# Performance work log

Hardware: AMD Instinct MI355X
Metric: run time of the kernel (lower is better)

## Reference

```python
import jax, jax.numpy as jnp
import numpy as np

D = 1024
H = 16
HD = D // H          # 64
D2 = D // 2          # 512
B = 2
N = 1024


def setup_inputs() -> dict:
    key = jax.random.key(0)
    ks = jax.random.split(key, 12)
    std = 0.02
    init_std = 0.02 / np.sqrt(D)  # matches _init_weights for value/output proj
    return {
        "h": jax.random.normal(ks[0], (B, N, D), jnp.float32),
        "prev_idx": jax.random.randint(ks[1], (B, N), 0, N),
        # forward encoders: Linear(d, d/2) -> GELU -> Linear(d/2, 1), stacked over heads
        "fw_W1": jax.random.normal(ks[2], (H, D2, D), jnp.float32) * std,
        "fw_b1": jnp.zeros((H, D2), jnp.float32),
        "fw_W2": jax.random.normal(ks[3], (H, D2), jnp.float32) * std,  # out-dim 1 squeezed
        "fw_b2": jnp.zeros((H,), jnp.float32),
        # backward encoders
        "bw_W1": jax.random.normal(ks[4], (H, D2, D), jnp.float32) * std,
        "bw_b1": jnp.zeros((H, D2), jnp.float32),
        "bw_W2": jax.random.normal(ks[5], (H, D2), jnp.float32) * std,
        "bw_b2": jnp.zeros((H,), jnp.float32),
        # per-head value projection Linear(d, head_dim, bias=False)
        "Wv": jax.random.normal(ks[6], (H, HD, D), jnp.float32) * init_std,
        # relation fusion: Linear(3*hd, hd) -> GELU -> Linear(hd, hd)
        "fu_W1": jax.random.normal(ks[7], (H, HD, 3 * HD), jnp.float32) * std,
        "fu_b1": jnp.zeros((H, HD), jnp.float32),
        "fu_W2": jax.random.normal(ks[8], (H, HD, HD), jnp.float32) * std,
        "fu_b2": jnp.zeros((H, HD), jnp.float32),
        # output projection Linear(d, d, bias=False)
        "Wo": jax.random.normal(ks[9], (D, D), jnp.float32) * init_std,
        "chain_ratio": jnp.float32(0.5),
    }


def _encoder_logits(h, W1, b1, W2, b2):
    # h: [B,N,D]; W1: [H,D2,D]; returns [H,B,N]
    x = jnp.einsum('bnd,hkd->hbnk', h, W1) + b1[:, None, None, :]
    x = jax.nn.gelu(x, approximate=False)  # torch nn.GELU default = exact erf
    return jnp.einsum('hbnk,hk->hbn', x, W2) + b2[:, None, None]


def reference(h, prev_idx, fw_W1, fw_b1, fw_W2, fw_b2,
              bw_W1, bw_b1, bw_W2, bw_b2,
              Wv, fu_W1, fu_b1, fu_W2, fu_b2, Wo, chain_ratio):
    pos = jnp.arange(N, dtype=h.dtype)

    fwd_logits = _encoder_logits(h, fw_W1, fw_b1, fw_W2, fw_b2)  # [H,B,N]
    bwd_logits = _encoder_logits(h, bw_W1, bw_b1, bw_W2, bw_b2)  # [H,B,N]

    # faithful to original: softmax over an N-wise expansion of a scalar logit
    fwd_probs = jax.nn.softmax(
        jnp.broadcast_to(fwd_logits[..., None], (H, B, N, N)), axis=-1)
    bwd_probs = jax.nn.softmax(
        jnp.broadcast_to(bwd_logits[..., None], (H, B, N, N)), axis=-1)

    fwd_targets = jnp.sum(fwd_probs * pos, axis=-1).astype(jnp.int32)  # [H,B,N]
    bwd_targets = jnp.sum(bwd_probs * pos, axis=-1).astype(jnp.int32)

    # chaining with prev_idx (prev_idx is given)
    chain_threshold = jnp.floor(jax.nn.sigmoid(chain_ratio) * N)
    should_chain = jnp.arange(N) >= chain_threshold  # [N]
    prev_clamped = jnp.clip(prev_idx, 0, N - 1).astype(jnp.int32)  # [B,N]
    fwd_targets = jnp.where(should_chain[None, None, :],
                            prev_clamped[None, :, :], fwd_targets)

    head_features = jnp.einsum('bnd,hed->hbne', h, Wv)  # [H,B,N,HD]
    fwd_feats = jnp.einsum('hbnm,hbme->hbne', fwd_probs, head_features)
    bwd_feats = jnp.einsum('hbnm,hbme->hbne', bwd_probs, head_features)

    rel = jnp.concatenate([head_features, fwd_feats, bwd_feats], axis=-1)  # [H,B,N,3HD]
    x = jax.nn.gelu(jnp.einsum('hbnc,hec->hbne', rel, fu_W1)
                    + fu_b1[:, None, None, :], approximate=False)
    head_out = jnp.einsum('hbne,hfe->hbnf', x, fu_W2) + fu_b2[:, None, None, :]

    multi = jnp.transpose(head_out, (1, 2, 0, 3)).reshape(B, N, D)
    final_output = jnp.einsum('bnd,ed->bne', multi, Wo)

    eps = 1e-8
    fwd_strength = 1.0 - jnp.sum(fwd_probs * jnp.log(fwd_probs + eps), axis=-1)
    bwd_strength = 1.0 - jnp.sum(bwd_probs * jnp.log(bwd_probs + eps), axis=-1)
    avg_strength = jnp.mean((fwd_strength + bwd_strength) * 0.5, axis=0)  # [B,N]

    return (final_output, fwd_targets[0], bwd_targets[0], avg_strength)
```

## Files before the change

kernel.cpp:

```cpp
#include <hip/hip_runtime.h>
#include <hip/hip_bf16.h>


typedef __attribute__((ext_vector_type(8))) short bf16x8;
typedef __attribute__((ext_vector_type(4))) float f32x4;

#define OFF_HBF  0
#define OFF_XBF  1048576
#define OFF_WVBF 2097152
#define OFF_MBF  2621440
#define OFF_W1A  3145728
#define OFF_HBAR 3178496
#define OFF_BIAS 3180544
#define OFF_C    3181568

__device__ __forceinline__ unsigned short f2bf(float f) {
    unsigned int u = __float_as_uint(f);
    u += 0x7fffu + ((u >> 16) & 1u);
    return (unsigned short)(u >> 16);
}

__device__ __forceinline__ void async_load16(const void* g, void* l) {
    __builtin_amdgcn_global_load_lds(
        (const __attribute__((address_space(1))) unsigned int*)g,
        (__attribute__((address_space(3))) unsigned int*)l, 16, 0, 0);
}

__global__ __launch_bounds__(256) void k_prep1(const float* __restrict__ h,
                                               const float* __restrict__ Wv,
                                               const float* __restrict__ fu_W1,
                                               unsigned short* __restrict__ hbf,
                                               unsigned short* __restrict__ Wvbf,
                                               unsigned short* __restrict__ W1abf,
                                               float* __restrict__ hbar) {
    int blk = blockIdx.x, tid = threadIdx.x;
    if (blk < 128) {
        int b = blk >> 6, chunk = blk & 63;
        int n0 = chunk * 16, d0 = tid * 4;
        const float* hb = h + (size_t)b * 1048576 + d0;
        unsigned short* ob = hbf + (size_t)b * 1048576 + d0;
        float4 sum = make_float4(0.f, 0.f, 0.f, 0.f);
#pragma unroll
        for (int i = 0; i < 16; ++i) {
            float4 v = *(const float4*)(hb + (size_t)(n0 + i) * 1024);
            sum.x += v.x; sum.y += v.y; sum.z += v.z; sum.w += v.w;
            *(ushort4*)(ob + (size_t)(n0 + i) * 1024) =
                make_ushort4(f2bf(v.x), f2bf(v.y), f2bf(v.z), f2bf(v.w));
        }
        float* hp = hbar + b * 1024 + d0;
        atomicAdd(hp + 0, sum.x * (1.f / 1024.f));
        atomicAdd(hp + 1, sum.y * (1.f / 1024.f));
        atomicAdd(hp + 2, sum.z * (1.f / 1024.f));
        atomicAdd(hp + 3, sum.w * (1.f / 1024.f));
    } else if (blk < 1152) {
        int i0 = (blk - 128) * 1024 + tid * 4;
        float4 v = *(const float4*)(Wv + i0);
        *(ushort4*)(Wvbf + i0) =
            make_ushort4(f2bf(v.x), f2bf(v.y), f2bf(v.z), f2bf(v.w));
    } else {
        int blk2 = blk - 1152;
        int hh = blk2 >> 2, q = blk2 & 3;
        int e = q * 16 + (tid >> 4);
        int k4 = (tid & 15) * 4;
        float4 v = *(const float4*)(fu_W1 + (size_t)(hh * 64 + e) * 192 + k4);
        *(ushort4*)(W1abf + hh * 4096 + e * 64 + k4) =
            make_ushort4(f2bf(v.x), f2bf(v.y), f2bf(v.z), f2bf(v.w));
    }
}

__global__ __launch_bounds__(256) void k_prep2(const float* __restrict__ Wo,
                                               const float* __restrict__ fu_W2,
                                               const float* __restrict__ fu_b2,
                                               const float* __restrict__ Wv,
                                               const float* __restrict__ fu_W1,
                                               const float* __restrict__ fu_b1,
                                               const float* __restrict__ hbar,
                                               unsigned short* __restrict__ Mbf,
                                               float* __restrict__ bias,
                                               float* __restrict__ cvec) {
    __shared__ float smem[8384];
    int blk = blockIdx.x, tid = threadIdx.x;
    if (blk < 256) {
        float* W2s = smem;
        float* Wos = smem + 4160;
        float* b2s = smem + 8320;
        int rc = blk >> 4, hh = blk & 15;
        int r0 = rc * 64;
#pragma unroll
        for (int i = 0; i < 16; ++i) {
            int idx = tid + i * 256;
            int f = idx >> 6, e = idx & 63;
            W2s[f * 65 + e] = fu_W2[hh * 4096 + idx];
            Wos[f * 65 + e] = Wo[(size_t)(r0 + f) * 1024 + hh * 64 + e];
        }
        if (tid < 64) b2s[tid] = fu_b2[hh * 64 + tid];
        __syncthreads();
        int ty = tid >> 3, tx = tid & 7;
        int r1 = 2 * ty, r2 = 2 * ty + 1, e0 = tx * 8;
        float acc0[8], acc1[8];
#pragma unroll
        for (int j = 0; j < 8; ++j) { acc0[j] = 0.f; acc1[j] = 0.f; }
        for (int f = 0; f < 64; ++f) {
            float a0 = Wos[r1 * 65 + f], a1 = Wos[r2 * 65 + f];
            const float* w2r = &W2s[f * 65 + e0];
#pragma unroll
            for (int j = 0; j < 8; ++j) {
                float b = w2r[j];
                acc0[j] += a0 * b;
                acc1[j] += a1 * b;
            }
        }
        unsigned short* m1 = Mbf + (size_t)(r0 + r1) * 1024 + hh * 64 + e0;
        unsigned short* m2 = Mbf + (size_t)(r0 + r2) * 1024 + hh * 64 + e0;
        *(ushort4*)(m1) = make_ushort4(f2bf(acc0[0]), f2bf(acc0[1]), f2bf(acc0[2]), f2bf(acc0[3]));
        *(ushort4*)(m1 + 4) = make_ushort4(f2bf(acc0[4]), f2bf(acc0[5]), f2bf(acc0[6]), f2bf(acc0[7]));
        *(ushort4*)(m2) = make_ushort4(f2bf(acc1[0]), f2bf(acc1[1]), f2bf(acc1[2]), f2bf(acc1[3]));
        *(ushort4*)(m2 + 4) = make_ushort4(f2bf(acc1[4]), f2bf(acc1[5]), f2bf(acc1[6]), f2bf(acc1[7]));
        if (tid < 64) {
            float p = 0.f;
#pragma unroll 8
            for (int f = 0; f < 64; ++f) p += Wos[tid * 65 + f] * b2s[f];
            atomicAdd(&bias[r0 + tid], p);
        }
    } else {
        float* psum = smem;
        float* mf = smem + 256;
        int blk2 = blk - 256;
        int b = blk2 >> 4, hh = blk2 & 15;
        int e = tid >> 2, sl = tid & 3;
        const float* wrow = Wv + (size_t)(hh * 64 + e) * 1024;
        const float* hb = hbar + b * 1024;
        float s = 0.f;
        int k0 = sl * 256;
        for (int k = k0; k < k0 + 256; ++k) s += wrow[k] * hb[k];
        psum[e * 4 + sl] = s;
        __syncthreads();
        if (tid < 64)
            mf[tid] = psum[tid * 4] + psum[tid * 4 + 1] + psum[tid * 4 + 2] + psum[tid * 4 + 3];
        __syncthreads();
        if (tid < 64) {
            const float* w1 = fu_W1 + (size_t)(hh * 64 + tid) * 192;
            float acc = fu_b1[hh * 64 + tid];
            for (int k = 0; k < 64; ++k) acc += (w1[64 + k] + w1[128 + k]) * mf[k];
            cvec[b * 1024 + hh * 64 + tid] = acc;
        }
    }
}

template <int MODE>
__global__ __launch_bounds__(256) void k_mm(const unsigned short* __restrict__ A,
                                            const unsigned short* __restrict__ Bw,
                                            void* __restrict__ CoutV,
                                            const unsigned short* __restrict__ W1a,
                                            const float* __restrict__ cvec,
                                            const float* __restrict__ bias,
                                            const int* __restrict__ prev_idx,
                                            const float* __restrict__ chain_ratio) {
    __shared__ __align__(16) char smem[12288];
    char* As = smem;
    char* Bs = smem + 4096;
    const int tid = threadIdx.x;
    const int w = tid >> 6, lane = tid & 63;
    const int rowBase = blockIdx.x * 32, colBase = blockIdx.y * 64;
    const int wmh = (w >> 1) * 16, wnh = (w & 1) * 32;
    const int lr = lane >> 3;
    const int ssrc = ((lane & 7) ^ lr) * 8;
    const int m_lane = lane & 15, quad = lane >> 4;

    if (MODE == 0 && blockIdx.x == 0 && blockIdx.y == 0) {
        float* out = (float*)CoutV;
        float cr = chain_ratio[0];
        float thr = floorf(1024.0f / (1.0f + expf(-cr)));
        float strength = 1.0f - logf(1.0f / 1024.0f + 1e-8f);
        for (int i = tid; i < 2048; i += 256) {
            int n = i & 1023;
            float fwd = 511.0f;
            if ((float)n >= thr) {
                int p = prev_idx[i];
                p = p < 0 ? 0 : (p > 1023 ? 1023 : p);
                fwd = (float)p;
            }
            out[2097152 + i] = fwd;
            out[2097152 + 2048 + i] = 511.0f;
            out[2097152 + 4096 + i] = strength;
        }
    }

    const unsigned short* Ag = A + (size_t)(rowBase + w * 8 + lr) * 1024 + ssrc;
    const unsigned short* Bg0 = Bw + (size_t)(colBase + w * 8 + lr) * 1024 + ssrc;
    const unsigned short* Bg1 = Bg0 + (size_t)32 * 1024;
    char* AsW = As + w * 1024;
    char* BsW = Bs + w * 1024;

    f32x4 acc[2];
    acc[0] = (f32x4){0.f, 0.f, 0.f, 0.f};
    acc[1] = (f32x4){0.f, 0.f, 0.f, 0.f};

    for (int k0 = 0; k0 < 1024; k0 += 64) {
        __syncthreads();
        async_load16(Ag + k0, AsW);
        async_load16(Bg0 + k0, BsW);
        async_load16(Bg1 + k0, BsW + 4096);
        __syncthreads();
#pragma unroll
        for (int kh = 0; kh < 2; ++kh) {
            const int seg = kh * 4 + quad;
            const int m = wmh + m_lane;
            bf16x8 af = *(const bf16x8*)(As + m * 128 + ((seg ^ (m & 7)) << 4));
#pragma unroll
            for (int nt = 0; nt < 2; ++nt) {
                int n = wnh + nt * 16 + m_lane;
                bf16x8 bfr = *(const bf16x8*)(Bs + n * 128 + ((seg ^ (n & 7)) << 4));
                acc[nt] = __builtin_amdgcn_mfma_f32_16x16x32_bf16(af, bfr, acc[nt], 0, 0, 0);
            }
        }
    }

    if (MODE == 0) {
        float* out = (float*)CoutV;
        float* Os = (float*)smem;
        __syncthreads();
#pragma unroll
        for (int nt = 0; nt < 2; ++nt) {
            int c = wnh + nt * 16 + m_lane;
            float bj = bias[colBase + c];
#pragma unroll
            for (int r4 = 0; r4 < 4; ++r4) {
                int r = wmh + quad * 4 + r4;
                Os[r * 68 + c] = acc[nt][r4] + bj;
            }
        }
        __syncthreads();
#pragma unroll
        for (int j = 0; j < 2; ++j) {
            int sidx = tid + j * 256;
            int r = sidx >> 4, sc = sidx & 15;
            float4 v = *(const float4*)&Os[r * 68 + sc * 4];
            *(float4*)&out[(size_t)(rowBase + r) * 1024 + colBase + sc * 4] = v;
        }
    } else {
        unsigned short* Xbf = (unsigned short*)CoutV;
        const int hh = blockIdx.y;
        __syncthreads();
        const unsigned short* Wg = W1a + hh * 4096 + (w * 8 + lr) * 64 + ssrc;
        async_load16(Wg, BsW);
        async_load16(Wg + 32 * 64, BsW + 4096);
#pragma unroll
        for (int nt = 0; nt < 2; ++nt) {
            int c = wnh + nt * 16 + m_lane;
#pragma unroll
            for (int r4 = 0; r4 < 4; ++r4) {
                int r = wmh + quad * 4 + r4;
                *(unsigned short*)(As + r * 128 + (((c >> 3) ^ (r & 7)) << 4) +
                                   (c & 7) * 2) = f2bf(acc[nt][r4]);
            }
        }
        __syncthreads();
        f32x4 acc2[2];
        acc2[0] = (f32x4){0.f, 0.f, 0.f, 0.f};
        acc2[1] = (f32x4){0.f, 0.f, 0.f, 0.f};
#pragma unroll
        for (int kh = 0; kh < 2; ++kh) {
            const int seg = kh * 4 + quad;
            const int m = wmh + m_lane;
            bf16x8 af = *(const bf16x8*)(As + m * 128 + ((seg ^ (m & 7)) << 4));
#pragma unroll
            for (int nt = 0; nt < 2; ++nt) {
                int n = wnh + nt * 16 + m_lane;
                bf16x8 bfr = *(const bf16x8*)(Bs + n * 128 + ((seg ^ (n & 7)) << 4));
                acc2[nt] = __builtin_amdgcn_mfma_f32_16x16x32_bf16(af, bfr, acc2[nt], 0, 0, 0);
            }
        }
        __syncthreads();
        const int b = rowBase >> 10;
#pragma unroll
        for (int nt = 0; nt < 2; ++nt) {
            int c = wnh + nt * 16 + m_lane;
            float cadd = cvec[b * 1024 + hh * 64 + c];
#pragma unroll
            for (int r4 = 0; r4 < 4; ++r4) {
                int r = wmh + quad * 4 + r4;
                float t = acc2[nt][r4] + cadd;
                t = 0.5f * t * (1.0f + erff(t * 0.70710678118654752f));
                *(unsigned short*)(As + r * 128 + c * 2) = f2bf(t);
            }
        }
        __syncthreads();
        int r = tid >> 3, s = tid & 7;
        float4 v = *(const float4*)(As + r * 128 + s * 16);
        *(float4*)((char*)Xbf + ((size_t)(rowBase + r) * 1024 + colBase + s * 8) * 2) = v;
    }
}

extern "C" void kernel_launch(void* const* d_in, const int* in_sizes, int n_in,
                              void* d_out, int out_size, void* d_ws, size_t ws_size,
                              hipStream_t stream) {
    const float* h      = (const float*)d_in[0];
    const int*   prev   = (const int*)d_in[1];
    const float* Wv     = (const float*)d_in[10];
    const float* fu_W1  = (const float*)d_in[11];
    const float* fu_b1  = (const float*)d_in[12];
    const float* fu_W2  = (const float*)d_in[13];
    const float* fu_b2  = (const float*)d_in[14];
    const float* Wo     = (const float*)d_in[15];
    const float* cratio = (const float*)d_in[16];

    float* out = (float*)d_out;
    float* ws  = (float*)d_ws;
    unsigned short* hbf   = (unsigned short*)(ws + OFF_HBF);
    unsigned short* Xbf   = (unsigned short*)(ws + OFF_XBF);
    unsigned short* Wvbf  = (unsigned short*)(ws + OFF_WVBF);
    unsigned short* Mbf   = (unsigned short*)(ws + OFF_MBF);
    unsigned short* W1abf = (unsigned short*)(ws + OFF_W1A);
    float* hbar = ws + OFF_HBAR;
    float* bias = ws + OFF_BIAS;
    float* cv   = ws + OFF_C;

    hipMemsetAsync(hbar, 0, 3072 * sizeof(float), stream);
    k_prep1<<<1216, 256, 0, stream>>>(h, Wv, fu_W1, hbf, Wvbf, W1abf, hbar);
    k_prep2<<<288, 256, 0, stream>>>(Wo, fu_W2, fu_b2, Wv, fu_W1, fu_b1, hbar,
                                     Mbf, bias, cv);
    k_mm<1><<<dim3(64, 16), 256, 0, stream>>>(hbf, Wvbf, Xbf, W1abf, cv,
                                              nullptr, nullptr, nullptr);
    k_mm<0><<<dim3(64, 16), 256, 0, stream>>>(Xbf, Mbf, out, nullptr, nullptr,
                                              bias, prev, cratio);
}
```

Measured before the change: 177.3 us.

## Enlarge GEMM row tile to 64 and restructure prep kernels without atomics

```diff
diff --git a/kernel.cpp b/kernel.cpp
--- a/kernel.cpp
+++ b/kernel.cpp
@@ -26,124 +26,155 @@
         (__attribute__((address_space(3))) unsigned int*)l, 16, 0, 0);
 }
 
-__global__ __launch_bounds__(256) void k_prep1(const float* __restrict__ h,
-                                               const float* __restrict__ Wv,
-                                               const float* __restrict__ fu_W1,
-                                               unsigned short* __restrict__ hbf,
-                                               unsigned short* __restrict__ Wvbf,
-                                               unsigned short* __restrict__ W1abf,
-                                               float* __restrict__ hbar) {
+__global__ __launch_bounds__(256) void k_prep(const float* __restrict__ h,
+                                              const float* __restrict__ Wv,
+                                              const float* __restrict__ fu_W1,
+                                              const float* __restrict__ Wo,
+                                              const float* __restrict__ fu_W2,
+                                              const float* __restrict__ fu_b2,
+                                              unsigned short* __restrict__ hbf,
+                                              unsigned short* __restrict__ Wvbf,
+                                              unsigned short* __restrict__ W1abf,
+                                              unsigned short* __restrict__ Mbf,
+                                              float* __restrict__ hbar,
+                                              float* __restrict__ bias) {
+    __shared__ float smem[8384];
     int blk = blockIdx.x, tid = threadIdx.x;
     if (blk < 128) {
         int b = blk >> 6, chunk = blk & 63;
         int n0 = chunk * 16, d0 = tid * 4;
         const float* hb = h + (size_t)b * 1048576 + d0;
         unsigned short* ob = hbf + (size_t)b * 1048576 + d0;
-        float4 sum = make_float4(0.f, 0.f, 0.f, 0.f);
 #pragma unroll
         for (int i = 0; i < 16; ++i) {
             float4 v = *(const float4*)(hb + (size_t)(n0 + i) * 1024);
-            sum.x += v.x; sum.y += v.y; sum.z += v.z; sum.w += v.w;
             *(ushort4*)(ob + (size_t)(n0 + i) * 1024) =
                 make_ushort4(f2bf(v.x), f2bf(v.y), f2bf(v.z), f2bf(v.w));
         }
-        float* hp = hbar + b * 1024 + d0;
-        atomicAdd(hp + 0, sum.x * (1.f / 1024.f));
-        atomicAdd(hp + 1, sum.y * (1.f / 1024.f));
-        atomicAdd(hp + 2, sum.z * (1.f / 1024.f));
-        atomicAdd(hp + 3, sum.w * (1.f / 1024.f));
-    } else if (blk < 1152) {
-        int i0 = (blk - 128) * 1024 + tid * 4;
-        float4 v = *(const float4*)(Wv + i0);
-        *(ushort4*)(Wvbf + i0) =
-            make_ushort4(f2bf(v.x), f2bf(v.y), f2bf(v.z), f2bf(v.w));
-    } else {
-        int blk2 = blk - 1152;
+    } else if (blk < 160) {
+        f32x4* psum = (f32x4*)smem;
+        int blk2 = blk - 128;
+        int b = blk2 >> 4, chunk = blk2 & 15;
+        int c0 = chunk * 64 + (tid & 15) * 4;
+        int ns = tid >> 4;
+        const float* hb = h + (size_t)b * 1048576 + c0;
+        float4 s = make_float4(0.f, 0.f, 0.f, 0.f);
+        for (int i = 0; i < 64; ++i) {
+            float4 v = *(const float4*)(hb + (size_t)(ns * 64 + i) * 1024);
+            s.x += v.x; s.y += v.y; s.z += v.z; s.w += v.w;
+        }
+        psum[(tid & 15) * 16 + ns] = (f32x4){s.x, s.y, s.z, s.w};
+        __syncthreads();
+        if (tid < 16) {
+            f32x4 a = (f32x4){0.f, 0.f, 0.f, 0.f};
+#pragma unroll
+            for (int j = 0; j < 16; ++j) a += psum[tid * 16 + j];
+            a *= (1.0f / 1024.0f);
+            *(float4*)(hbar + b * 1024 + chunk * 64 + tid * 4) =
+                make_float4(a[0], a[1], a[2], a[3]);
+        }
+    } else if (blk < 416) {
+        float* W2s = smem;
+        float* Wos = smem + 4160;
+        int blk2 = blk - 160;
+        int rc = blk2 >> 4, hh = blk2 & 15;
+        int r0 = rc * 64;
+#pragma unroll
+        for (int i = 0; i < 16; ++i) {
+            int idx = tid + i * 256;
+            int f = idx >> 6, e = idx & 63;
+            W2s[f * 65 + e] = fu_W2[hh * 4096 + idx];
+            Wos[f * 65 + e] = Wo[(size_t)(r0 + f) * 1024 + hh * 64 + e];
+        }
+        __syncthreads();
+        int ty = tid >> 3, tx = tid & 7;
+        int r1 = 2 * ty, r2 = 2 * ty + 1, e0 = tx * 8;
+        float acc0[8], acc1[8];
+#pragma unroll
+        for (int j = 0; j < 8; ++j) { acc0[j] = 0.f; acc1[j] = 0.f; }
+        for (int f = 0; f < 64; ++f) {
+            float a0 = Wos[r1 * 65 + f], a1 = Wos[r2 * 65 + f];
+            const float* w2r = &W2s[f * 65 + e0];
+#pragma unroll
+            for (int j = 0; j < 8; ++j) {
+                float b = w2r[j];
+                acc0[j] += a0 * b;
+                acc1[j] += a1 * b;
+            }
+        }
+        unsigned short* m1 = Mbf + (size_t)(r0 + r1) * 1024 + hh * 64 + e0;
+        unsigned short* m2 = Mbf + (size_t)(r0 + r2) * 1024 + hh * 64 + e0;
+        *(ushort4*)(m1) = make_ushort4(f2bf(acc0[0]), f2bf(acc0[1]), f2bf(acc0[2]), f2bf(acc0[3]));
+        *(ushort4*)(m1 + 4) = make_ushort4(f2bf(acc0[4]), f2bf(acc0[5]), f2bf(acc0[6]), f2bf(acc0[7]));
+        *(ushort4*)(m2) = make_ushort4(f2bf(acc1[0]), f2bf(acc1[1]), f2bf(acc1[2]), f2bf(acc1[3]));
+        *(ushort4*)(m2 + 4) = make_ushort4(f2bf(acc1[4]), f2bf(acc1[5]), f2bf(acc1[6]), f2bf(acc1[7]));
+    } else if (blk < 432) {
+        float* b2s = smem;
+        *(float4*)(b2s + tid * 4) = *(const float4*)(fu_b2 + tid * 4);
+        __syncthreads();
+        int r0 = (blk - 416) * 64;
+        int w = tid >> 6, lane = tid & 63;
+        int c0 = lane * 16;
+#pragma unroll
+        for (int g = 0; g < 16; ++g) {
+            int r = r0 + g * 4 + w;
+            const float* wo = Wo + (size_t)r * 1024 + c0;
+            float p = 0.f;
+#pragma unroll
+            for (int j = 0; j < 4; ++j) {
+                float4 a = *(const float4*)(wo + j * 4);
+                float4 b = *(const float4*)(b2s + c0 + j * 4);
+                p += a.x * b.x + a.y * b.y + a.z * b.z + a.w * b.w;
+            }
+#pragma unroll
+            for (int off = 32; off > 0; off >>= 1) p += __shfl_down(p, off, 64);
+            if (lane == 0) bias[r] = p;
+        }
+    } else if (blk < 496) {
+        int blk2 = blk - 432;
         int hh = blk2 >> 2, q = blk2 & 3;
         int e = q * 16 + (tid >> 4);
         int k4 = (tid & 15) * 4;
         float4 v = *(const float4*)(fu_W1 + (size_t)(hh * 64 + e) * 192 + k4);
         *(ushort4*)(W1abf + hh * 4096 + e * 64 + k4) =
             make_ushort4(f2bf(v.x), f2bf(v.y), f2bf(v.z), f2bf(v.w));
-    }
-}
-
-__global__ __launch_bounds__(256) void k_prep2(const float* __restrict__ Wo,
-                                               const float* __restrict__ fu_W2,
-                                               const float* __restrict__ fu_b2,
-                                               const float* __restrict__ Wv,
-                                               const float* __restrict__ fu_W1,
-                                               const float* __restrict__ fu_b1,
-                                               const float* __restrict__ hbar,
-                                               unsigned short* __restrict__ Mbf,
-                                               float* __restrict__ bias,
-                                               float* __restrict__ cvec) {
-    __shared__ float smem[8384];
-    int blk = blockIdx.x, tid = threadIdx.x;
-    if (blk < 256) {
-        float* W2s = smem;
-        float* Wos = smem + 4160;
-        float* b2s = smem + 8320;
-        int rc = blk >> 4, hh = blk & 15;
-        int r0 = rc * 64;
-#pragma unroll
-        for (int i = 0; i < 16; ++i) {
-            int idx = tid + i * 256;
-            int f = idx >> 6, e = idx & 63;
-            W2s[f * 65 + e] = fu_W2[hh * 4096 + idx];
-            Wos[f * 65 + e] = Wo[(size_t)(r0 + f) * 1024 + hh * 64 + e];
-        }
-        if (tid < 64) b2s[tid] = fu_b2[hh * 64 + tid];
-        __syncthreads();
-        int ty = tid >> 3, tx = tid & 7;
-        int r1 = 2 * ty, r2 = 2 * ty + 1, e0 = tx * 8;
-        float acc0[8], acc1[8];
-#pragma unroll
-        for (int j = 0; j < 8; ++j) { acc0[j] = 0.f; acc1[j] = 0.f; }
-        for (int f = 0; f < 64; ++f) {
-            float a0 = Wos[r1 * 65 + f], a1 = Wos[r2 * 65 + f];
-            const float* w2r = &W2s[f * 65 + e0];
-#pragma unroll
-            for (int j = 0; j < 8; ++j) {
-                float b = w2r[j];
-                acc0[j] += a0 * b;
-                acc1[j] += a1 * b;
-            }
-        }
-        unsigned short* m1 = Mbf + (size_t)(r0 + r1) * 1024 + hh * 64 + e0;
-        unsigned short* m2 = Mbf + (size_t)(r0 + r2) * 1024 + hh * 64 + e0;
-        *(ushort4*)(m1) = make_ushort4(f2bf(acc0[0]), f2bf(acc0[1]), f2bf(acc0[2]), f2bf(acc0[3]));
-        *(ushort4*)(m1 + 4) = make_ushort4(f2bf(acc0[4]), f2bf(acc0[5]), f2bf(acc0[6]), f2bf(acc0[7]));
-        *(ushort4*)(m2) = make_ushort4(f2bf(acc1[0]), f2bf(acc1[1]), f2bf(acc1[2]), f2bf(acc1[3]));
-        *(ushort4*)(m2 + 4) = make_ushort4(f2bf(acc1[4]), f2bf(acc1[5]), f2bf(acc1[6]), f2bf(acc1[7]));
-        if (tid < 64) {
-            float p = 0.f;
-#pragma unroll 8
-            for (int f = 0; f < 64; ++f) p += Wos[tid * 65 + f] * b2s[f];
-            atomicAdd(&bias[r0 + tid], p);
-        }
     } else {
-        float* psum = smem;
-        float* mf = smem + 256;
-        int blk2 = blk - 256;
-        int b = blk2 >> 4, hh = blk2 & 15;
-        int e = tid >> 2, sl = tid & 3;
-        const float* wrow = Wv + (size_t)(hh * 64 + e) * 1024;
-        const float* hb = hbar + b * 1024;
-        float s = 0.f;
-        int k0 = sl * 256;
-        for (int k = k0; k < k0 + 256; ++k) s += wrow[k] * hb[k];
-        psum[e * 4 + sl] = s;
-        __syncthreads();
-        if (tid < 64)
-            mf[tid] = psum[tid * 4] + psum[tid * 4 + 1] + psum[tid * 4 + 2] + psum[tid * 4 + 3];
-        __syncthreads();
-        if (tid < 64) {
-            const float* w1 = fu_W1 + (size_t)(hh * 64 + tid) * 192;
-            float acc = fu_b1[hh * 64 + tid];
-            for (int k = 0; k < 64; ++k) acc += (w1[64 + k] + w1[128 + k]) * mf[k];
-            cvec[b * 1024 + hh * 64 + tid] = acc;
-        }
+        int base = (blk - 496) * 4096;
+#pragma unroll
+        for (int j = 0; j < 4; ++j) {
+            int i0 = base + j * 1024 + tid * 4;
+            float4 v = *(const float4*)(Wv + i0);
+            *(ushort4*)(Wvbf + i0) =
+                make_ushort4(f2bf(v.x), f2bf(v.y), f2bf(v.z), f2bf(v.w));
+        }
+    }
+}
+
+__global__ __launch_bounds__(256) void k_cvec(const float* __restrict__ Wv,
+                                              const float* __restrict__ fu_W1,
+                                              const float* __restrict__ fu_b1,
+                                              const float* __restrict__ hbar,
+                                              float* __restrict__ cvec) {
+    __shared__ float psum[256];
+    __shared__ float mf[64];
+    int b = blockIdx.x >> 4, hh = blockIdx.x & 15;
+    int tid = threadIdx.x;
+    int e = tid >> 2, sl = tid & 3;
+    const float* wrow = Wv + (size_t)(hh * 64 + e) * 1024;
+    const float* hb = hbar + b * 1024;
+    float s = 0.f;
+    int k0 = sl * 256;
+    for (int k = k0; k < k0 + 256; ++k) s += wrow[k] * hb[k];
+    psum[e * 4 + sl] = s;
+    __syncthreads();
+    if (tid < 64)
+        mf[tid] = psum[tid * 4] + psum[tid * 4 + 1] + psum[tid * 4 + 2] + psum[tid * 4 + 3];
+    __syncthreads();
+    if (tid < 64) {
+        const float* w1 = fu_W1 + (size_t)(hh * 64 + tid) * 192;
+        float acc = fu_b1[hh * 64 + tid];
+        for (int k = 0; k < 64; ++k) acc += (w1[64 + k] + w1[128 + k]) * mf[k];
+        cvec[b * 1024 + hh * 64 + tid] = acc;
     }
 }
 
@@ -156,13 +187,13 @@
                                             const float* __restrict__ bias,
                                             const int* __restrict__ prev_idx,
                                             const float* __restrict__ chain_ratio) {
-    __shared__ __align__(16) char smem[12288];
+    __shared__ __align__(16) char smem[17408];
     char* As = smem;
-    char* Bs = smem + 4096;
+    char* Bs = smem + 8192;
     const int tid = threadIdx.x;
     const int w = tid >> 6, lane = tid & 63;
-    const int rowBase = blockIdx.x * 32, colBase = blockIdx.y * 64;
-    const int wmh = (w >> 1) * 16, wnh = (w & 1) * 32;
+    const int rowBase = blockIdx.x * 64, colBase = blockIdx.y * 64;
+    const int wmh = (w >> 1) * 32, wnh = (w & 1) * 32;
     const int lr = lane >> 3;
     const int ssrc = ((lane & 7) ^ lr) * 8;
     const int m_lane = lane & 15, quad = lane >> 4;
@@ -186,33 +217,46 @@
         }
     }
 
-    const unsigned short* Ag = A + (size_t)(rowBase + w * 8 + lr) * 1024 + ssrc;
+    const unsigned short* Ag0 = A + (size_t)(rowBase + w * 8 + lr) * 1024 + ssrc;
+    const unsigned short* Ag1 = Ag0 + (size_t)32 * 1024;
     const unsigned short* Bg0 = Bw + (size_t)(colBase + w * 8 + lr) * 1024 + ssrc;
     const unsigned short* Bg1 = Bg0 + (size_t)32 * 1024;
     char* AsW = As + w * 1024;
     char* BsW = Bs + w * 1024;
 
-    f32x4 acc[2];
-    acc[0] = (f32x4){0.f, 0.f, 0.f, 0.f};
-    acc[1] = (f32x4){0.f, 0.f, 0.f, 0.f};
+    f32x4 acc[2][2];
+#pragma unroll
+    for (int i = 0; i < 2; ++i)
+#pragma unroll
+        for (int j = 0; j < 2; ++j) acc[i][j] = (f32x4){0.f, 0.f, 0.f, 0.f};
 
     for (int k0 = 0; k0 < 1024; k0 += 64) {
         __syncthreads();
-        async_load16(Ag + k0, AsW);
+        async_load16(Ag0 + k0, AsW);
+        async_load16(Ag1 + k0, AsW + 4096);
         async_load16(Bg0 + k0, BsW);
         async_load16(Bg1 + k0, BsW + 4096);
         __syncthreads();
 #pragma unroll
         for (int kh = 0; kh < 2; ++kh) {
             const int seg = kh * 4 + quad;
-            const int m = wmh + m_lane;
-            bf16x8 af = *(const bf16x8*)(As + m * 128 + ((seg ^ (m & 7)) << 4));
+            bf16x8 af[2], bfr[2];
+#pragma unroll
+            for (int mt = 0; mt < 2; ++mt) {
+                int m = wmh + mt * 16 + m_lane;
+                af[mt] = *(const bf16x8*)(As + m * 128 + ((seg ^ (m & 7)) << 4));
+            }
 #pragma unroll
             for (int nt = 0; nt < 2; ++nt) {
                 int n = wnh + nt * 16 + m_lane;
-                bf16x8 bfr = *(const bf16x8*)(Bs + n * 128 + ((seg ^ (n & 7)) << 4));
-                acc[nt] = __builtin_amdgcn_mfma_f32_16x16x32_bf16(af, bfr, acc[nt], 0, 0, 0);
-            }
+                bfr[nt] = *(const bf16x8*)(Bs + n * 128 + ((seg ^ (n & 7)) << 4));
+            }
+#pragma unroll
+            for (int mt = 0; mt < 2; ++mt)
+#pragma unroll
+                for (int nt = 0; nt < 2; ++nt)
+                    acc[mt][nt] = __builtin_amdgcn_mfma_f32_16x16x32_bf16(
+                        af[mt], bfr[nt], acc[mt][nt], 0, 0, 0);
         }
     }
 
@@ -225,14 +269,16 @@
             int c = wnh + nt * 16 + m_lane;
             float bj = bias[colBase + c];
 #pragma unroll
-            for (int r4 = 0; r4 < 4; ++r4) {
-                int r = wmh + quad * 4 + r4;
-                Os[r * 68 + c] = acc[nt][r4] + bj;
-            }
-        }
-        __syncthreads();
-#pragma unroll
-        for (int j = 0; j < 2; ++j) {
+            for (int mt = 0; mt < 2; ++mt)
+#pragma unroll
+                for (int r4 = 0; r4 < 4; ++r4) {
+                    int r = wmh + mt * 16 + quad * 4 + r4;
+                    Os[r * 68 + c] = acc[mt][nt][r4] + bj;
+                }
+        }
+        __syncthreads();
+#pragma unroll
+        for (int j = 0; j < 4; ++j) {
             int sidx = tid + j * 256;
             int r = sidx >> 4, sc = sidx & 15;
             float4 v = *(const float4*)&Os[r * 68 + sc * 4];
@@ -246,49 +292,69 @@
         async_load16(Wg, BsW);
         async_load16(Wg + 32 * 64, BsW + 4096);
 #pragma unroll
-        for (int nt = 0; nt < 2; ++nt) {
-            int c = wnh + nt * 16 + m_lane;
-#pragma unroll
-            for (int r4 = 0; r4 < 4; ++r4) {
-                int r = wmh + quad * 4 + r4;
-                *(unsigned short*)(As + r * 128 + (((c >> 3) ^ (r & 7)) << 4) +
-                                   (c & 7) * 2) = f2bf(acc[nt][r4]);
-            }
-        }
-        __syncthreads();
-        f32x4 acc2[2];
-        acc2[0] = (f32x4){0.f, 0.f, 0.f, 0.f};
-        acc2[1] = (f32x4){0.f, 0.f, 0.f, 0.f};
+        for (int mt = 0; mt < 2; ++mt)
+#pragma unroll
+            for (int nt = 0; nt < 2; ++nt) {
+                int c = wnh + nt * 16 + m_lane;
+#pragma unroll
+                for (int r4 = 0; r4 < 4; ++r4) {
+                    int r = wmh + mt * 16 + quad * 4 + r4;
+                    *(unsigned short*)(As + r * 128 + (((c >> 3) ^ (r & 7)) << 4) +
+                                       (c & 7) * 2) = f2bf(acc[mt][nt][r4]);
+                }
+            }
+        __syncthreads();
+        f32x4 acc2[2][2];
+#pragma unroll
+        for (int i = 0; i < 2; ++i)
+#pragma unroll
+            for (int j = 0; j < 2; ++j) acc2[i][j] = (f32x4){0.f, 0.f, 0.f, 0.f};
 #pragma unroll
         for (int kh = 0; kh < 2; ++kh) {
             const int seg = kh * 4 + quad;
-            const int m = wmh + m_lane;
-            bf16x8 af = *(const bf16x8*)(As + m * 128 + ((seg ^ (m & 7)) << 4));
+            bf16x8 af[2], bfr[2];
+#pragma unroll
+            for (int mt = 0; mt < 2; ++mt) {
+                int m = wmh + mt * 16 + m_lane;
+                af[mt] = *(const bf16x8*)(As + m * 128 + ((seg ^ (m & 7)) << 4));
+            }
 #pragma unroll
             for (int nt = 0; nt < 2; ++nt) {
                 int n = wnh + nt * 16 + m_lane;
-                bf16x8 bfr = *(const bf16x8*)(Bs + n * 128 + ((seg ^ (n & 7)) << 4));
-                acc2[nt] = __builtin_amdgcn_mfma_f32_16x16x32_bf16(af, bfr, acc2[nt], 0, 0, 0);
-            }
+                bfr[nt] = *(const bf16x8*)(Bs + n * 128 + ((seg ^ (n & 7)) << 4));
+            }
+#pragma unroll
+            for (int mt = 0; mt < 2; ++mt)
+#pragma unroll
+                for (int nt = 0; nt < 2; ++nt)
+                    acc2[mt][nt] = __builtin_amdgcn_mfma_f32_16x16x32_bf16(
+                        af[mt], bfr[nt], acc2[mt][nt], 0, 0, 0);
         }
         __syncthreads();
         const int b = rowBase >> 10;
 #pragma unroll
-        for (int nt = 0; nt < 2; ++nt) {
-            int c = wnh + nt * 16 + m_lane;
-            float cadd = cvec[b * 1024 + hh * 64 + c];
-#pragma unroll
-            for (int r4 = 0; r4 < 4; ++r4) {
-                int r = wmh + quad * 4 + r4;
-                float t = acc2[nt][r4] + cadd;
-                t = 0.5f * t * (1.0f + erff(t * 0.70710678118654752f));
-                *(unsigned short*)(As + r * 128 + c * 2) = f2bf(t);
-            }
-        }
-        __syncthreads();
-        int r = tid >> 3, s = tid & 7;
-        float4 v = *(const float4*)(As + r * 128 + s * 16);
-        *(float4*)((char*)Xbf + ((size_t)(rowBase + r) * 1024 + colBase + s * 8) * 2) = v;
+        for (int mt = 0; mt < 2; ++mt)
+#pragma unroll
+            for (int nt = 0; nt < 2; ++nt) {
+                int c = wnh + nt * 16 + m_lane;
+                float cadd = cvec[b * 1024 + hh * 64 + c];
+#pragma unroll
+                for (int r4 = 0; r4 < 4; ++r4) {
+                    int r = wmh + mt * 16 + quad * 4 + r4;
+                    float t = acc2[mt][nt][r4] + cadd;
+                    t = 0.5f * t * (1.0f + erff(t * 0.70710678118654752f));
+                    *(unsigned short*)(As + r * 128 + c * 2) = f2bf(t);
+                }
+            }
+        __syncthreads();
+#pragma unroll
+        for (int j = 0; j < 2; ++j) {
+            int seg = tid + j * 256;
+            int r = seg >> 3, s = seg & 7;
+            float4 v = *(const float4*)(As + r * 128 + s * 16);
+            *(float4*)((char*)Xbf +
+                       ((size_t)(rowBase + r) * 1024 + colBase + s * 8) * 2) = v;
+        }
     }
 }
 
@@ -316,12 +382,11 @@
     float* bias = ws + OFF_BIAS;
     float* cv   = ws + OFF_C;
 
-    hipMemsetAsync(hbar, 0, 3072 * sizeof(float), stream);
-    k_prep1<<<1216, 256, 0, stream>>>(h, Wv, fu_W1, hbf, Wvbf, W1abf, hbar);
-    k_prep2<<<288, 256, 0, stream>>>(Wo, fu_W2, fu_b2, Wv, fu_W1, fu_b1, hbar,
-                                     Mbf, bias, cv);
-    k_mm<1><<<dim3(64, 16), 256, 0, stream>>>(hbf, Wvbf, Xbf, W1abf, cv,
+    k_prep<<<752, 256, 0, stream>>>(h, Wv, fu_W1, Wo, fu_W2, fu_b2,
+                                    hbf, Wvbf, W1abf, Mbf, hbar, bias);
+    k_cvec<<<32, 256, 0, stream>>>(Wv, fu_W1, fu_b1, hbar, cv);
+    k_mm<1><<<dim3(32, 16), 256, 0, stream>>>(hbf, Wvbf, Xbf, W1abf, cv,
                                               nullptr, nullptr, nullptr);
-    k_mm<0><<<dim3(64, 16), 256, 0, stream>>>(Xbf, Mbf, out, nullptr, nullptr,
+    k_mm<0><<<dim3(32, 16), 256, 0, stream>>>(Xbf, Mbf, out, nullptr, nullptr,
                                               bias, prev, cratio);
 }
```

New measurement: 179.2 us. Within noise of the previous version (+1.1%).
